# Kernel tuning notes

Measured on AMD Instinct MI355X. Metric: run time of the kernel, lower is better.

The kernel has to match this reference:

```python
import jax, jax.numpy as jnp
import numpy as np

HEADS = 16
HIDDEN = 1024
DH = HIDDEN // HEADS
STD = 0.02


def setup_inputs() -> dict:
    key = jax.random.key(0)
    ks = jax.random.split(key, 12)
    B, S = 4, 2048
    inp = {
        'q': jax.random.normal(ks[0], (B, S, HIDDEN), jnp.float32),
        'k': jax.random.normal(ks[1], (B, S, HIDDEN), jnp.float32),
        'v': jax.random.normal(ks[2], (B, S, HIDDEN), jnp.float32),
        'mask': jax.random.randint(ks[3], (B, S), 0, 2, jnp.int32),
        # linear layers: weight [out,in] torch-style, init N(0, 0.02), bias 0
        'wq': STD * jax.random.normal(ks[4], (HIDDEN, HIDDEN), jnp.float32),
        'bq': jnp.zeros((HIDDEN,), jnp.float32),
        'wk': STD * jax.random.normal(ks[5], (HIDDEN, HIDDEN), jnp.float32),
        'bk': jnp.zeros((HIDDEN,), jnp.float32),
        'wv': STD * jax.random.normal(ks[6], (HIDDEN, HIDDEN), jnp.float32),
        'bv': jnp.zeros((HIDDEN,), jnp.float32),
        'wo': STD * jax.random.normal(ks[7], (HIDDEN, HIDDEN), jnp.float32),
        'bo': jnp.zeros((HIDDEN,), jnp.float32),
    }
    return inp


def _split_heads(x):
    B, S, _ = x.shape
    return x.reshape(B, S, HEADS, DH).transpose(0, 2, 1, 3)  # [B,H,S,dh]


def reference(q, k, v, mask, wq, bq, wk, bk, wv, bv, wo, bo):
    B, S, _ = q.shape
    qh = _split_heads(q @ wq.T + bq)
    kh = _split_heads(k @ wk.T + bk)
    vh = _split_heads(v @ wv.T + bv)
    scale = 1.0 / jnp.sqrt(jnp.float32(DH))
    corr = jnp.einsum('bhqd,bhkd->bhqk', qh, kh) * scale  # [B,H,S,S]
    # original masks QUERY rows: mask [B,S] -> [B,1,S,1] broadcast over heads & keys
    row_mask = (mask != 0)[:, None, :, None]
    corr = jnp.where(row_mask, corr, jnp.float32(-1e9))
    prob = jax.nn.softmax(corr, axis=-1)
    # dropout p=0.0 (eval / deterministic reference)
    hidden = jnp.einsum('bhqk,bhkd->bhqd', prob, vh)
    hidden = hidden.transpose(0, 2, 1, 3).reshape(B, S, HIDDEN)
    return hidden @ wo.T + bo
```

## Files before the change

kernel.cpp:

```cpp
#include <hip/hip_runtime.h>

#define BATCH 4
#define SEQ 2048
#define HEADS 16
#define DHEAD 64
#define HID 1024
#define MROWS (BATCH * SEQ)
#define QSCALE 0.1803368801111092f

typedef unsigned short u16;
typedef unsigned int u32;
typedef __attribute__((ext_vector_type(4))) float f32x4;
typedef __attribute__((ext_vector_type(8))) short bf16x8;
typedef __attribute__((ext_vector_type(2))) unsigned int u32x2;

#define MFMA16(a, b, c) __builtin_amdgcn_mfma_f32_16x16x32_bf16((a), (b), (c), 0, 0, 0)
#define EXP2F(x) __builtin_amdgcn_exp2f(x)

__device__ __forceinline__ u16 f2bf(float f) {
  union { float f; u32 i; } x; x.f = f;
  u32 r = x.i + 0x7fffu + ((x.i >> 16) & 1u);
  return (u16)(r >> 16);
}

__device__ __forceinline__ u32 cvtpk(float a, float b) {
  u32 d;
  asm("v_cvt_pk_bf16_f32 %0, %1, %2" : "=v"(d) : "v"(a), "v"(b));
  return d;
}

__device__ __forceinline__ void lds16(const u16* g, u16* s) {
  __builtin_amdgcn_global_load_lds(
      (const __attribute__((address_space(1))) void*)g,
      (__attribute__((address_space(3))) void*)s, 16, 0, 0);
}

__device__ __forceinline__ void stage8f(const float* __restrict__ g, u16* s) {
  const float4 a = *(const float4*)g;
  const float4 b = *(const float4*)(g + 4);
  ushort4 lo, hi;
  lo.x = f2bf(a.x); lo.y = f2bf(a.y); lo.z = f2bf(a.z); lo.w = f2bf(a.w);
  hi.x = f2bf(b.x); hi.y = f2bf(b.y); hi.z = f2bf(b.z); hi.w = f2bf(b.w);
  *(ushort4*)s = lo;
  *(ushort4*)(s + 4) = hi;
}

struct CvtArgs {
  const float* src[7];
  u16* dst[7];
};
__global__ __launch_bounds__(256) void cvt7(CvtArgs args, int yoff, int nact) {
  const int y = blockIdx.y + yoff;
  const int i = (blockIdx.x * 256 + threadIdx.x) * 8;
  if (y < 3) {
    if (i < nact) stage8f(args.src[y] + i, args.dst[y] + i);
  } else {
    if (i < 4 * (1 << 20)) {
      const int j = i >> 20, off = i & ((1 << 20) - 1);
      stage8f(args.src[3 + j] + off, args.dst[3 + j] + off);
    }
  }
}

template<bool ADMA, bool BDMA>
__device__ __forceinline__ void gemm_core(
    const void* __restrict__ Av, const void* __restrict__ Wv,
    int tid, int m0, int n0, u16* As, u16* Bs, f32x4 (&acc)[4][4])
{
  const int srow = tid >> 2, cslot = tid & 3;
  const int gc = cslot ^ ((srow >> 1) & 3);
  const int w = tid >> 6, l = tid & 63;
  const int quad = l >> 4, l15 = l & 15;
  const int sw = (l15 >> 1) & 3;
  const int wm = (w & 1) << 6, wn = (w >> 1) << 6;

  for (int k0 = 0; k0 < HID; k0 += 32) {
    if (ADMA) {
      const u16* ag = (const u16*)Av + (size_t)(m0 + srow) * HID + k0 + gc * 8;
      lds16(ag, &As[tid * 8]);
      lds16(ag + (size_t)64 * HID, &As[2048 + tid * 8]);
    } else {
      const float* ag = (const float*)Av + (size_t)(m0 + srow) * HID + k0 + gc * 8;
      stage8f(ag, &As[srow * 32 + cslot * 8]);
      stage8f(ag + (size_t)64 * HID, &As[(64 + srow) * 32 + cslot * 8]);
    }
    if (BDMA) {
      const u16* bg = (const u16*)Wv + (size_t)(n0 + srow) * HID + k0 + gc * 8;
      lds16(bg, &Bs[tid * 8]);
      lds16(bg + (size_t)64 * HID, &Bs[2048 + tid * 8]);
    } else {
      const float* bg = (const float*)Wv + (size_t)(n0 + srow) * HID + k0 + gc * 8;
      stage8f(bg, &Bs[srow * 32 + cslot * 8]);
      stage8f(bg + (size_t)64 * HID, &Bs[(64 + srow) * 32 + cslot * 8]);
    }
    __syncthreads();

    bf16x8 a[4], b[4];
    #pragma unroll
    for (int i = 0; i < 4; ++i)
      a[i] = *(const bf16x8*)&As[(wm + i * 16 + l15) * 32 + (quad ^ sw) * 8];
    #pragma unroll
    for (int j = 0; j < 4; ++j)
      b[j] = *(const bf16x8*)&Bs[(wn + j * 16 + l15) * 32 + (quad ^ sw) * 8];
    #pragma unroll
    for (int i = 0; i < 4; ++i)
      #pragma unroll
      for (int j = 0; j < 4; ++j)
        acc[i][j] = MFMA16(a[i], b[j], acc[i][j]);
    __syncthreads();
  }
}

template<bool ADMA, bool BDMA>
__global__ __launch_bounds__(256) void gemm_qkv(
    const void* __restrict__ xq, const void* __restrict__ xk,
    const void* __restrict__ xv,
    const void* __restrict__ wqv, const void* __restrict__ wkv,
    const void* __restrict__ wvv,
    const float* __restrict__ bq, const float* __restrict__ bk,
    const float* __restrict__ bv, const int* __restrict__ Mask,
    u16* __restrict__ qh, u16* __restrict__ kh, u16* __restrict__ vt)
{
  __shared__ u16 As[128 * 32];
  __shared__ u16 Bs[128 * 32];
  const int z = blockIdx.z;
  const void* A = (z == 0) ? xq : (z == 1) ? xk : xv;
  const void* W = (z == 0) ? wqv : (z == 1) ? wkv : wvv;
  const float* Bias = (z == 0) ? bq : (z == 1) ? bk : bv;

  const int tid = threadIdx.x;
  const int m0 = blockIdx.x << 7, n0 = blockIdx.y << 7;
  f32x4 acc[4][4] = {};
  gemm_core<ADMA, BDMA>(A, W, tid, m0, n0, As, Bs, acc);

  const int w = tid >> 6, l = tid & 63;
  const int quad = l >> 4, l15 = l & 15;
  const int wm = (w & 1) << 6, wn = (w >> 1) << 6;

  if (z <= 1) {
    u16* Out = (z == 0) ? qh : kh;
    #pragma unroll
    for (int i = 0; i < 4; ++i) {
      float fl[4];
      #pragma unroll
      for (int r = 0; r < 4; ++r) {
        const int m = m0 + wm + i * 16 + (quad << 2) + r;
        fl[r] = (z == 0) ? (Mask[m] ? QSCALE : 0.f) : 1.f;
      }
      #pragma unroll
      for (int j = 0; j < 4; ++j) {
        const int n = n0 + wn + j * 16 + l15;
        const float bias = Bias[n];
        const int h = n >> 6, d = n & 63;
        #pragma unroll
        for (int r = 0; r < 4; ++r) {
          const int m = m0 + wm + i * 16 + (quad << 2) + r;
          const int bb = m >> 11, s = m & (SEQ - 1);
          Out[((size_t)(bb * HEADS + h) * SEQ + s) * DHEAD + d] =
              f2bf((acc[i][j][r] + bias) * fl[r]);
        }
      }
    }
  } else {
    const int sblk = (m0 + wm) & (SEQ - 1);
    const int bb = (m0 + wm) >> 11;
    #pragma unroll
    for (int j = 0; j < 4; ++j) {
      const int n = n0 + wn + j * 16 + l15;
      const float bias = Bias[n];
      const int h = n >> 6, d = n & 63;
      u16* base = vt + ((size_t)(bb * HEADS + h) * DHEAD + d) * SEQ + sblk;
      #pragma unroll
      for (int r = 0; r < 4; ++r) {
        u32x2 pk;
        pk.x = cvtpk(acc[0][j][r] + bias, acc[1][j][r] + bias);
        pk.y = cvtpk(acc[2][j][r] + bias, acc[3][j][r] + bias);
        *(u32x2*)(base + ((quad << 2) + r) * 4) = pk;
      }
    }
  }
}

template<bool BDMA>
__global__ __launch_bounds__(256) void gemm_out(
    const u16* __restrict__ hidden, const void* __restrict__ wov,
    const float* __restrict__ bo, float* __restrict__ Out)
{
  __shared__ u16 As[128 * 32];
  __shared__ u16 Bs[128 * 32];
  const int tid = threadIdx.x;
  const int m0 = blockIdx.x << 7, n0 = blockIdx.y << 7;
  f32x4 acc[4][4] = {};
  gemm_core<true, BDMA>(hidden, wov, tid, m0, n0, As, Bs, acc);

  const int w = tid >> 6, l = tid & 63;
  const int quad = l >> 4, l15 = l & 15;
  const int wm = (w & 1) << 6, wn = (w >> 1) << 6;
  #pragma unroll
  for (int j = 0; j < 4; ++j) {
    const int n = n0 + wn + j * 16 + l15;
    const float bias = bo[n];
    #pragma unroll
    for (int i = 0; i < 4; ++i) {
      const int mb = m0 + wm + i * 16 + (quad << 2);
      #pragma unroll
      for (int r = 0; r < 4; ++r)
        Out[(size_t)(mb + r) * HID + n] = acc[i][j][r] + bias;
    }
  }
}

__global__ __launch_bounds__(128, 2) void attn_mfma(
    const u16* __restrict__ QH, const u16* __restrict__ KH,
    const u16* __restrict__ VT, u16* __restrict__ Hidden)
{
  __shared__ u16 QP[128 * 64];
  __shared__ u16 Ks[2][2048];
  __shared__ u16 Vt[2][2][2048];

  const int tid = threadIdx.x;
  const int w = tid >> 6, l = tid & 63;
  const int quad = l >> 4, l15 = l & 15;
  const int sw = (l15 >> 1) & 3;
  const int srow = tid >> 2, cslot = tid & 3;
  const int gc = cslot ^ ((srow >> 1) & 3);

  const int lin = blockIdx.y * 16 + blockIdx.x;
  const int bh = lin & 63, b = bh >> 4, h = bh & 15;
  const int q0 = (lin >> 6) << 7;

  const u16* qbase = QH + (size_t)bh * SEQ * DHEAD;
  const u16* kbase = KH + (size_t)bh * SEQ * DHEAD;
  const u16* vbase = VT + (size_t)bh * DHEAD * SEQ;

  #pragma unroll
  for (int hh = 0; hh < 2; ++hh)
    #pragma unroll
    for (int part = 0; part < 4; ++part)
      lds16(qbase + (size_t)(q0 + part * 32 + srow) * DHEAD + hh * 32 + gc * 8,
            &QP[hh * 4096 + part * 1024 + tid * 8]);
  #pragma unroll
  for (int hh = 0; hh < 2; ++hh)
    #pragma unroll
    for (int part = 0; part < 2; ++part)
      lds16(kbase + (size_t)(part * 32 + srow) * DHEAD + hh * 32 + gc * 8,
            &Ks[hh][part * 1024 + tid * 8]);
  #pragma unroll
  for (int hh = 0; hh < 2; ++hh)
    #pragma unroll
    for (int part = 0; part < 2; ++part)
      lds16(vbase + (size_t)(part * 32 + srow) * SEQ + hh * 32 + gc * 8,
            &Vt[0][hh][part * 1024 + tid * 8]);
  asm volatile("s_waitcnt vmcnt(8)" ::: "memory");
  __builtin_amdgcn_s_barrier();

  bf16x8 aq[2][4];
  #pragma unroll
  for (int hh = 0; hh < 2; ++hh)
    #pragma unroll
    for (int i = 0; i < 4; ++i)
      aq[hh][i] = *(const bf16x8*)
          &QP[hh * 4096 + (w * 64 + i * 16 + l15) * 32 + (quad ^ sw) * 8];

  float lsum[4][4] = {};
  f32x4 o[4][4] = {};
  int cur = 0;

  for (int it = 0; it < SEQ / 64; ++it) {
    asm volatile("s_waitcnt vmcnt(4)" ::: "memory");
    __builtin_amdgcn_s_barrier();

    f32x4 s[4][4] = {};
    __builtin_amdgcn_s_setprio(1);
    #pragma unroll
    for (int j = 0; j < 4; ++j)
      #pragma unroll
      for (int hh = 0; hh < 2; ++hh) {
        const bf16x8 bk = *(const bf16x8*)
            &Ks[hh][(j * 16 + l15) * 32 + (quad ^ sw) * 8];
        #pragma unroll
        for (int i = 0; i < 4; ++i)
          s[i][j] = MFMA16(aq[hh][i], bk, s[i][j]);
      }
    __builtin_amdgcn_s_setprio(0);
    __builtin_amdgcn_s_barrier();

    const int tn = ((it + 1) & (SEQ / 64 - 1)) << 6;
    #pragma unroll
    for (int hh = 0; hh < 2; ++hh)
      #pragma unroll
      for (int part = 0; part < 2; ++part)
        lds16(kbase + (size_t)(tn + part * 32 + srow) * DHEAD + hh * 32 + gc * 8,
              &Ks[hh][part * 1024 + tid * 8]);
    #pragma unroll
    for (int hh = 0; hh < 2; ++hh)
      #pragma unroll
      for (int part = 0; part < 2; ++part)
        lds16(vbase + (size_t)(part * 32 + srow) * SEQ + tn + hh * 32 + gc * 8,
              &Vt[cur ^ 1][hh][part * 1024 + tid * 8]);

    #pragma unroll
    for (int i = 0; i < 4; ++i)
      #pragma unroll
      for (int r = 0; r < 4; ++r) {
        const float p0 = EXP2F(s[i][0][r]);
        const float p1 = EXP2F(s[i][1][r]);
        const float p2 = EXP2F(s[i][2][r]);
        const float p3 = EXP2F(s[i][3][r]);
        lsum[i][r] += (p0 + p1) + (p2 + p3);
        const int row = w * 64 + i * 16 + (quad << 2) + r;
        const int cs = ((l15 >> 1) ^ (row & 7)) * 8 + (l15 & 1) * 4;
        u32x2 pk;
        pk.x = cvtpk(p0, p1);
        pk.y = cvtpk(p2, p3);
        *(u32x2*)&QP[row * 64 + cs] = pk;
      }

    asm volatile("s_waitcnt vmcnt(8)" ::: "memory");
    __builtin_amdgcn_s_barrier();

    __builtin_amdgcn_s_setprio(1);
    #pragma unroll
    for (int hh = 0; hh < 2; ++hh) {
      bf16x8 ap[4];
      #pragma unroll
      for (int i = 0; i < 4; ++i) {
        const int row = w * 64 + i * 16 + l15;
        ap[i] = *(const bf16x8*)
            &QP[row * 64 + (((hh * 4 + quad) ^ (row & 7)) << 3)];
      }
      #pragma unroll
      for (int j = 0; j < 4; ++j) {
        const bf16x8 vb = *(const bf16x8*)
            &Vt[cur][hh][(j * 16 + l15) * 32 + (quad ^ sw) * 8];
        #pragma unroll
        for (int i = 0; i < 4; ++i)
          o[i][j] = MFMA16(ap[i], vb, o[i][j]);
      }
    }
    __builtin_amdgcn_s_setprio(0);
    cur ^= 1;
  }
  asm volatile("s_waitcnt vmcnt(0)" ::: "memory");

  float inv[4][4];
  #pragma unroll
  for (int i = 0; i < 4; ++i)
    #pragma unroll
    for (int r = 0; r < 4; ++r) {
      float t = lsum[i][r];
      #pragma unroll
      for (int off = 1; off < 16; off <<= 1)
        t += __shfl_xor(t, off);
      inv[i][r] = 1.f / t;
    }

  #pragma unroll
  for (int i = 0; i < 4; ++i)
    #pragma unroll
    for (int j = 0; j < 4; ++j)
      #pragma unroll
      for (int r = 0; r < 4; ++r) {
        const int qrow = q0 + w * 64 + i * 16 + (quad << 2) + r;
        Hidden[((size_t)(b * SEQ + qrow)) * HID + h * DHEAD + j * 16 + l15] =
            f2bf(o[i][j][r] * inv[i][r]);
      }
}

extern "C" void kernel_launch(void* const* d_in, const int* in_sizes, int n_in,
                              void* d_out, int out_size, void* d_ws, size_t ws_size,
                              hipStream_t stream) {
  const float* q  = (const float*)d_in[0];
  const float* k  = (const float*)d_in[1];
  const float* v  = (const float*)d_in[2];
  const int* mask = (const int*)d_in[3];
  const float* wq = (const float*)d_in[4];
  const float* bq = (const float*)d_in[5];
  const float* wk = (const float*)d_in[6];
  const float* bk = (const float*)d_in[7];
  const float* wv = (const float*)d_in[8];
  const float* bv = (const float*)d_in[9];
  const float* wo = (const float*)d_in[10];
  const float* bo = (const float*)d_in[11];

  const size_t SEG = (size_t)MROWS * HID;
  const size_t WSEG = (size_t)HID * HID;
  const dim3 gq(MROWS / 128, HID / 128, 3);
  const dim3 go(MROWS / 128, HID / 128);
  const dim3 ga(SEQ / 128, BATCH * HEADS);

  const size_t planFULL = (6 * SEG + 4 * WSEG) * sizeof(u16);
  const size_t planMID  = (4 * SEG + 4 * WSEG) * sizeof(u16);

  if (ws_size >= planFULL) {
    u16* qb  = (u16*)d_ws;
    u16* kb  = qb + SEG;
    u16* vb  = kb + SEG;
    u16* qh  = vb + SEG;
    u16* kh  = qh + SEG;
    u16* vt  = kh + SEG;
    u16* wqb = vt + SEG;
    u16* wkb = wqb + WSEG;
    u16* wvb = wkb + WSEG;
    u16* wob = wvb + WSEG;
    u16* hidden = qb;

    CvtArgs ca;
    ca.src[0] = q;  ca.dst[0] = qb;
    ca.src[1] = k;  ca.dst[1] = kb;
    ca.src[2] = v;  ca.dst[2] = vb;
    ca.src[3] = wq; ca.dst[3] = wqb;
    ca.src[4] = wk; ca.dst[4] = wkb;
    ca.src[5] = wv; ca.dst[5] = wvb;
    ca.src[6] = wo; ca.dst[6] = wob;
    cvt7<<<dim3(SEG / 2048, 4), 256, 0, stream>>>(ca, 0, (int)SEG);

    gemm_qkv<true, true><<<gq, 256, 0, stream>>>(qb, kb, vb, wqb, wkb, wvb,
                                                 bq, bk, bv, mask, qh, kh, vt);
    attn_mfma<<<ga, 128, 0, stream>>>(qh, kh, vt, hidden);
    gemm_out<true><<<go, 256, 0, stream>>>(hidden, wob, bo, (float*)d_out);
  } else if (ws_size >= planMID) {
    u16* wqb = (u16*)d_ws;
    u16* wkb = wqb + WSEG;
    u16* wvb = wkb + WSEG;
    u16* wob = wvb + WSEG;
    u16* qh = wob + WSEG;
    u16* kh = qh + SEG;
    u16* vt = kh + SEG;
    u16* hidden = vt + SEG;

    CvtArgs ca;
    ca.src[0] = ca.src[1] = ca.src[2] = q;
    ca.dst[0] = ca.dst[1] = ca.dst[2] = wqb;
    ca.src[3] = wq; ca.dst[3] = wqb;
    ca.src[4] = wk; ca.dst[4] = wkb;
    ca.src[5] = wv; ca.dst[5] = wvb;
    ca.src[6] = wo; ca.dst[6] = wob;
    cvt7<<<dim3(4 * WSEG / 2048, 1), 256, 0, stream>>>(ca, 3, 0);

    gemm_qkv<false, true><<<gq, 256, 0, stream>>>(q, k, v, wqb, wkb, wvb,
                                                  bq, bk, bv, mask, qh, kh, vt);
    attn_mfma<<<ga, 128, 0, stream>>>(qh, kh, vt, hidden);
    gemm_out<true><<<go, 256, 0, stream>>>(hidden, wob, bo, (float*)d_out);
  } else {
    u16* qh = (u16*)d_ws;
    u16* kh = qh + SEG;
    u16* vt = kh + SEG;
    u16* hidden = vt + SEG;

    gemm_qkv<false, false><<<gq, 256, 0, stream>>>(q, k, v, wq, wk, wv,
                                                   bq, bk, bv, mask, qh, kh, vt);
    attn_mfma<<<ga, 128, 0, stream>>>(qh, kh, vt, hidden);
    gemm_out<false><<<go, 256, 0, stream>>>(hidden, wo, bo, (float*)d_out);
  }
}
```

Measured before the change: 343.0 us.

## Compute transposed S^T so P stays in registers, row sums via MFMA

The attention kernel now computes S^T = K·Q^T, so each lane's exp'd probabilities are already laid out as the B operand of the PV MFMA. The P tile no longer round-trips through LDS, which drops one LDS write/read phase per iteration. The V tile is loaded with a new swizzled layout so O^T = V^T·P^T can be formed directly. Row sums come from an extra MFMA against a ones vector instead of VALU adds and shuffles, and the output is stored as packed bf16 pairs. The cost is extra MFMA work for the sums, and the sums now use bf16-rounded probabilities.

```diff
diff --git a/kernel.cpp b/kernel.cpp
--- a/kernel.cpp
+++ b/kernel.cpp
@@ -13,6 +13,7 @@
 typedef __attribute__((ext_vector_type(4))) float f32x4;
 typedef __attribute__((ext_vector_type(8))) short bf16x8;
 typedef __attribute__((ext_vector_type(2))) unsigned int u32x2;
+typedef __attribute__((ext_vector_type(4))) unsigned int u32x4;
 
 #define MFMA16(a, b, c) __builtin_amdgcn_mfma_f32_16x16x32_bf16((a), (b), (c), 0, 0, 0)
 #define EXP2F(x) __builtin_amdgcn_exp2f(x)
@@ -214,9 +215,9 @@
     const u16* __restrict__ QH, const u16* __restrict__ KH,
     const u16* __restrict__ VT, u16* __restrict__ Hidden)
 {
-  __shared__ u16 QP[128 * 64];
+  __shared__ u16 Qs[2][128 * 32];
   __shared__ u16 Ks[2][2048];
-  __shared__ u16 Vt[2][2][2048];
+  __shared__ u16 Vt[2][4096];
 
   const int tid = threadIdx.x;
   const int w = tid >> 6, l = tid & 63;
@@ -224,6 +225,8 @@
   const int sw = (l15 >> 1) & 3;
   const int srow = tid >> 2, cslot = tid & 3;
   const int gc = cslot ^ ((srow >> 1) & 3);
+  const int vd = tid >> 3;
+  const int vc = (tid & 7) ^ (vd & 7);
 
   const int lin = blockIdx.y * 16 + blockIdx.x;
   const int bh = lin & 63, b = bh >> 4, h = bh & 15;
@@ -238,7 +241,7 @@
     #pragma unroll
     for (int part = 0; part < 4; ++part)
       lds16(qbase + (size_t)(q0 + part * 32 + srow) * DHEAD + hh * 32 + gc * 8,
-            &QP[hh * 4096 + part * 1024 + tid * 8]);
+            &Qs[hh][part * 1024 + tid * 8]);
   #pragma unroll
   for (int hh = 0; hh < 2; ++hh)
     #pragma unroll
@@ -246,11 +249,9 @@
       lds16(kbase + (size_t)(part * 32 + srow) * DHEAD + hh * 32 + gc * 8,
             &Ks[hh][part * 1024 + tid * 8]);
   #pragma unroll
-  for (int hh = 0; hh < 2; ++hh)
-    #pragma unroll
-    for (int part = 0; part < 2; ++part)
-      lds16(vbase + (size_t)(part * 32 + srow) * SEQ + hh * 32 + gc * 8,
-            &Vt[0][hh][part * 1024 + tid * 8]);
+  for (int part = 0; part < 4; ++part)
+    lds16(vbase + (size_t)(part * 16 + vd) * SEQ + vc * 8,
+          &Vt[0][part * 1024 + tid * 8]);
   asm volatile("s_waitcnt vmcnt(8)" ::: "memory");
   __builtin_amdgcn_s_barrier();
 
@@ -258,12 +259,14 @@
   #pragma unroll
   for (int hh = 0; hh < 2; ++hh)
     #pragma unroll
-    for (int i = 0; i < 4; ++i)
-      aq[hh][i] = *(const bf16x8*)
-          &QP[hh * 4096 + (w * 64 + i * 16 + l15) * 32 + (quad ^ sw) * 8];
-
-  float lsum[4][4] = {};
+    for (int j = 0; j < 4; ++j)
+      aq[hh][j] = *(const bf16x8*)
+          &Qs[hh][(w * 64 + j * 16 + l15) * 32 + (quad ^ sw) * 8];
+
+  const bf16x8 ones8 = {0x3F80, 0x3F80, 0x3F80, 0x3F80,
+                        0x3F80, 0x3F80, 0x3F80, 0x3F80};
   f32x4 o[4][4] = {};
+  f32x4 lacc[4] = {};
   int cur = 0;
 
   for (int it = 0; it < SEQ / 64; ++it) {
@@ -273,14 +276,14 @@
     f32x4 s[4][4] = {};
     __builtin_amdgcn_s_setprio(1);
     #pragma unroll
-    for (int j = 0; j < 4; ++j)
+    for (int i = 0; i < 4; ++i)
       #pragma unroll
       for (int hh = 0; hh < 2; ++hh) {
-        const bf16x8 bk = *(const bf16x8*)
-            &Ks[hh][(j * 16 + l15) * 32 + (quad ^ sw) * 8];
+        const bf16x8 ak = *(const bf16x8*)
+            &Ks[hh][(i * 16 + l15) * 32 + (quad ^ sw) * 8];
         #pragma unroll
-        for (int i = 0; i < 4; ++i)
-          s[i][j] = MFMA16(aq[hh][i], bk, s[i][j]);
+        for (int j = 0; j < 4; ++j)
+          s[i][j] = MFMA16(ak, aq[hh][j], s[i][j]);
       }
     __builtin_amdgcn_s_setprio(0);
     __builtin_amdgcn_s_barrier();
@@ -293,78 +296,65 @@
         lds16(kbase + (size_t)(tn + part * 32 + srow) * DHEAD + hh * 32 + gc * 8,
               &Ks[hh][part * 1024 + tid * 8]);
     #pragma unroll
-    for (int hh = 0; hh < 2; ++hh)
-      #pragma unroll
-      for (int part = 0; part < 2; ++part)
-        lds16(vbase + (size_t)(part * 32 + srow) * SEQ + tn + hh * 32 + gc * 8,
-              &Vt[cur ^ 1][hh][part * 1024 + tid * 8]);
-
-    #pragma unroll
-    for (int i = 0; i < 4; ++i)
-      #pragma unroll
-      for (int r = 0; r < 4; ++r) {
-        const float p0 = EXP2F(s[i][0][r]);
-        const float p1 = EXP2F(s[i][1][r]);
-        const float p2 = EXP2F(s[i][2][r]);
-        const float p3 = EXP2F(s[i][3][r]);
-        lsum[i][r] += (p0 + p1) + (p2 + p3);
-        const int row = w * 64 + i * 16 + (quad << 2) + r;
-        const int cs = ((l15 >> 1) ^ (row & 7)) * 8 + (l15 & 1) * 4;
-        u32x2 pk;
-        pk.x = cvtpk(p0, p1);
-        pk.y = cvtpk(p2, p3);
-        *(u32x2*)&QP[row * 64 + cs] = pk;
-      }
+    for (int part = 0; part < 4; ++part)
+      lds16(vbase + (size_t)(part * 16 + vd) * SEQ + tn + vc * 8,
+            &Vt[cur ^ 1][part * 1024 + tid * 8]);
+
+    bf16x8 bp[2][4];
+    #pragma unroll
+    for (int j = 0; j < 4; ++j) {
+      float p[4][4];
+      #pragma unroll
+      for (int i = 0; i < 4; ++i)
+        #pragma unroll
+        for (int r = 0; r < 4; ++r)
+          p[i][r] = EXP2F(s[i][j][r]);
+      u32x4 t0, t1;
+      t0.x = cvtpk(p[0][0], p[1][0]); t0.y = cvtpk(p[2][0], p[3][0]);
+      t0.z = cvtpk(p[0][1], p[1][1]); t0.w = cvtpk(p[2][1], p[3][1]);
+      t1.x = cvtpk(p[0][2], p[1][2]); t1.y = cvtpk(p[2][2], p[3][2]);
+      t1.z = cvtpk(p[0][3], p[1][3]); t1.w = cvtpk(p[2][3], p[3][3]);
+      bp[0][j] = __builtin_bit_cast(bf16x8, t0);
+      bp[1][j] = __builtin_bit_cast(bf16x8, t1);
+      lacc[j] = MFMA16(ones8, bp[0][j], lacc[j]);
+      lacc[j] = MFMA16(ones8, bp[1][j], lacc[j]);
+    }
 
     asm volatile("s_waitcnt vmcnt(8)" ::: "memory");
     __builtin_amdgcn_s_barrier();
 
     __builtin_amdgcn_s_setprio(1);
     #pragma unroll
-    for (int hh = 0; hh < 2; ++hh) {
-      bf16x8 ap[4];
-      #pragma unroll
-      for (int i = 0; i < 4; ++i) {
-        const int row = w * 64 + i * 16 + l15;
-        ap[i] = *(const bf16x8*)
-            &QP[row * 64 + (((hh * 4 + quad) ^ (row & 7)) << 3)];
+    for (int hh = 0; hh < 2; ++hh)
+      #pragma unroll
+      for (int m = 0; m < 4; ++m) {
+        const int d = m * 16 + l15;
+        const bf16x8 av = *(const bf16x8*)
+            &Vt[cur][d * 64 + (((quad * 2 + hh) ^ (d & 7)) << 3)];
+        #pragma unroll
+        for (int j = 0; j < 4; ++j)
+          o[m][j] = MFMA16(av, bp[hh][j], o[m][j]);
       }
-      #pragma unroll
-      for (int j = 0; j < 4; ++j) {
-        const bf16x8 vb = *(const bf16x8*)
-            &Vt[cur][hh][(j * 16 + l15) * 32 + (quad ^ sw) * 8];
-        #pragma unroll
-        for (int i = 0; i < 4; ++i)
-          o[i][j] = MFMA16(ap[i], vb, o[i][j]);
-      }
-    }
     __builtin_amdgcn_s_setprio(0);
     cur ^= 1;
   }
   asm volatile("s_waitcnt vmcnt(0)" ::: "memory");
 
-  float inv[4][4];
-  #pragma unroll
-  for (int i = 0; i < 4; ++i)
-    #pragma unroll
-    for (int r = 0; r < 4; ++r) {
-      float t = lsum[i][r];
-      #pragma unroll
-      for (int off = 1; off < 16; off <<= 1)
-        t += __shfl_xor(t, off);
-      inv[i][r] = 1.f / t;
-    }
-
-  #pragma unroll
-  for (int i = 0; i < 4; ++i)
-    #pragma unroll
-    for (int j = 0; j < 4; ++j)
-      #pragma unroll
-      for (int r = 0; r < 4; ++r) {
-        const int qrow = q0 + w * 64 + i * 16 + (quad << 2) + r;
-        Hidden[((size_t)(b * SEQ + qrow)) * HID + h * DHEAD + j * 16 + l15] =
-            f2bf(o[i][j][r] * inv[i][r]);
-      }
+  float inv[4];
+  #pragma unroll
+  for (int j = 0; j < 4; ++j)
+    inv[j] = 1.f / lacc[j][0];
+
+  #pragma unroll
+  for (int m = 0; m < 4; ++m)
+    #pragma unroll
+    for (int j = 0; j < 4; ++j) {
+      u32x2 pk;
+      pk.x = cvtpk(o[m][j][0] * inv[j], o[m][j][1] * inv[j]);
+      pk.y = cvtpk(o[m][j][2] * inv[j], o[m][j][3] * inv[j]);
+      *(u32x2*)&Hidden[(size_t)(b * SEQ + q0 + w * 64 + j * 16 + l15) * HID
+                       + h * DHEAD + m * 16 + quad * 4] = pk;
+    }
 }
 
 extern "C" void kernel_launch(void* const* d_in, const int* in_sizes, int n_in,
```

New measurement: 328.9 us. -4.1%, faster.
